# Kernel tuning notes

Measured on AMD Instinct MI355X. Metric: run time of the kernel, lower is better.

Reference implementation:

```python
import jax, jax.numpy as jnp
import numpy as np

B, E, W_WORDS, V = 512, 512, 64, 32000
H = 10 * E  # dense hidden = embedding_size * 10


def setup_inputs() -> dict:
    key = jax.random.key(0)
    ks = jax.random.split(key, 16)
    u = lambda k, shp: jax.random.uniform(ks[k], shp, jnp.float32, -0.05, 0.05)
    n = lambda k, shp: jax.random.normal(ks[k], shp, jnp.float32)
    return {
        "y": n(0, (B, E)),
        "state": n(1, (B, E)),
        "encode": n(2, (B, W_WORDS, E)),
        # Bahdanau attention weights (W4 unused in forward, omitted)
        "aW1": u(3, (1, E)),
        "aW2": u(4, (W_WORDS, E)),
        "aW3": u(5, (W_WORDS, E)),
        # Keras GRU (reset_after=True): kernel, recurrent_kernel, bias[2, 3E]
        "gk": u(6, (E, 3 * E)),
        "grk": u(7, (E, 3 * E)),
        "gb": u(8, (2, 3 * E)),
        # Dense stack
        "w1": u(9, (3 * E, H)), "b1": jnp.zeros((H,), jnp.float32),
        "w2": u(10, (H, H)), "b2": jnp.zeros((H,), jnp.float32),
        "w3": u(11, (H, V)), "b3": jnp.zeros((V,), jnp.float32),
    }


def _attention(query, value, aW1, aW2, aW3):
    # einsum('bi,ci->bi', query, W1) with c==1  ->  query * W1[0]
    rq = query * aW1[0]                       # [B, E]
    rv = value * aW2                          # [B, W, E] (broadcast over batch)
    s = jnp.tanh(rq[:, None, :] * rv)         # [B, W, E]
    scores = jnp.sum(s * aW3, axis=-1)        # [B, W]
    a = jax.nn.softmax(scores, axis=-1)       # [B, W]
    return jnp.einsum('bw,bwe->be', a, value)  # context [B, E]


def _gru(seq, gk, grk, gb):
    # seq: [T, B, E]; keras GRU defaults: tanh / sigmoid, reset_after=True, h0=0
    bi, br = gb[0], gb[1]

    def step(h, x):
        xz, xr, xh = jnp.split(x @ gk + bi, 3, axis=-1)
        rz, rr, rh = jnp.split(h @ grk + br, 3, axis=-1)
        z = jax.nn.sigmoid(xz + rz)
        r = jax.nn.sigmoid(xr + rr)
        hh = jnp.tanh(xh + r * rh)
        return z * h + (1.0 - z) * hh, None

    h0 = jnp.zeros(seq.shape[1:], seq.dtype)
    h, _ = jax.lax.scan(step, h0, seq)
    return h


def reference(y, state, encode, aW1, aW2, aW3, gk, grk, gb, w1, b1, w2, b2, w3, b3):
    context = _attention(state, encode, aW1, aW2, aW3)   # [B, E]
    seq = jnp.stack([state, context, y], axis=0)          # [3, B, E]
    new_state = _gru(seq, gk, grk, gb)                    # [B, E]
    g = jnp.concatenate([y, context, new_state], axis=-1)  # [B, 3E]
    h1 = jnp.tanh(g @ w1 + b1)
    h2 = jnp.tanh(h1 @ w2 + b2)
    g_output = jax.nn.softmax(h2 @ w3 + b3, axis=-1)      # [B, V]
    return (g_output, new_state)
```

## Files before the change

### kernel.cpp

```cpp
#include <hip/hip_runtime.h>
#include <hip/hip_bf16.h>
#include <math.h>

#define B_DIM 512
#define E_DIM 512
#define W_DIM 64
#define V_DIM 32000
#define H_DIM 5120

typedef short bf16x8 __attribute__((ext_vector_type(8)));
typedef float f32x4 __attribute__((ext_vector_type(4)));

static __device__ __forceinline__ unsigned pk2(float a, float b) {
  union { __hip_bfloat16 h; unsigned short u; } ca, cb;
  ca.h = __float2bfloat16(a);
  cb.h = __float2bfloat16(b);
  return (unsigned)ca.u | ((unsigned)cb.u << 16);
}
static __device__ __forceinline__ unsigned short f2b(float a) {
  union { __hip_bfloat16 h; unsigned short u; } c;
  c.h = __float2bfloat16(a);
  return c.u;
}

__global__ __launch_bounds__(256) void attn_kernel(
    const float* __restrict__ state, const float* __restrict__ encode,
    const float* __restrict__ aW1, const float* __restrict__ aW2,
    const float* __restrict__ aW3, float* __restrict__ ctx) {
  const int b = blockIdx.x;
  const int tid = threadIdx.x;
  __shared__ float rq[512];
  __shared__ float sc[64];
  rq[tid]       = state[(size_t)b * 512 + tid]       * aW1[tid];
  rq[tid + 256] = state[(size_t)b * 512 + tid + 256] * aW1[tid + 256];
  __syncthreads();
  const int lane = tid & 63, wv = tid >> 6;
  const float* enc = encode + (size_t)b * 64 * 512;
  for (int w = wv; w < 64; w += 4) {
    const float* er  = enc + w * 512;
    const float* w2r = aW2 + w * 512;
    const float* w3r = aW3 + w * 512;
    float s = 0.f;
#pragma unroll
    for (int k = 0; k < 8; ++k) {
      int e = lane + k * 64;
      s += tanhf(rq[e] * er[e] * w2r[e]) * w3r[e];
    }
#pragma unroll
    for (int o = 32; o; o >>= 1) s += __shfl_xor(s, o, 64);
    if (lane == 0) sc[w] = s;
  }
  __syncthreads();
  if (tid < 64) {
    float v = sc[tid];
    float mx = v;
#pragma unroll
    for (int o = 32; o; o >>= 1) mx = fmaxf(mx, __shfl_xor(mx, o, 64));
    float e = __expf(v - mx);
    float sm = e;
#pragma unroll
    for (int o = 32; o; o >>= 1) sm += __shfl_xor(sm, o, 64);
    sc[tid] = e / sm;
  }
  __syncthreads();
  for (int e = tid; e < 512; e += 256) {
    float acc = 0.f;
#pragma unroll 8
    for (int w = 0; w < 64; ++w) acc += sc[w] * enc[w * 512 + e];
    ctx[(size_t)b * 512 + e] = acc;
  }
}

__global__ __launch_bounds__(256) void pack3(
    const float* __restrict__ s0, const float* __restrict__ s1,
    const float* __restrict__ s2, float* __restrict__ dst) {
  const int s = blockIdx.y;
  const int i = blockIdx.x * 256 + threadIdx.x;
  const float* src = (s == 0) ? s0 : ((s == 1) ? s1 : s2);
  dst[(size_t)s * 262144 + i] = src[i];
}

__global__ __launch_bounds__(256) void pack3b(
    const float* __restrict__ s0, const float* __restrict__ s1,
    const float* __restrict__ s2, unsigned short* __restrict__ dst) {
  const int s = blockIdx.y;
  const int i = blockIdx.x * 256 + threadIdx.x;
  const float* src = (s == 0) ? s0 : ((s == 1) ? s1 : s2);
  const int b = i >> 9, e = i & 511;
  dst[(size_t)b * 1536 + s * 512 + e] = f2b(src[i]);
}

__global__ __launch_bounds__(256) void gru_gate(
    const float* __restrict__ X, const float* __restrict__ R, int rstride,
    const float* __restrict__ hprev, float* __restrict__ hout) {
  const int i = blockIdx.x * 256 + threadIdx.x;
  const int b = i >> 9, e = i & 511;
  const float* Xr = X + (size_t)b * 1536;
  const float* Rr = R + (size_t)b * rstride;
  const float xz = Xr[e], xr = Xr[512 + e], xh = Xr[1024 + e];
  const float rz = Rr[e], rr = Rr[512 + e], rh = Rr[1024 + e];
  const float h = hprev ? hprev[i] : 0.f;
  const float z = 1.f / (1.f + __expf(-(xz + rz)));
  const float r = 1.f / (1.f + __expf(-(xr + rr)));
  const float hh = tanhf(xh + r * rh);
  hout[i] = z * h + (1.f - z) * hh;
}

template <int ACT>
__global__ __launch_bounds__(256, 2) void gemm_k(
    const float* __restrict__ A, const float* __restrict__ B,
    const float* __restrict__ bias, float* __restrict__ C,
    int M, int N, int K) {
  __shared__ unsigned short As[128 * 72];
  __shared__ unsigned short Bs[128 * 72];
  const int tid = threadIdx.x;
  const int bid = blockIdx.x;
  const int tiles_m = M >> 7;
  const int mt = bid % tiles_m;
  const int nt = bid / tiles_m;
  const long m0 = (long)mt * 128, n0 = (long)nt * 128;

  const int a_m = tid & 127;
  const int a_h = tid >> 7;
  unsigned short* awp = As + a_m * 72 + a_h * 32;
  const int b_n = (tid & 31) << 2;
  const int b_q = (tid >> 5) & 3;
  const int b_h = tid >> 7;
  const int b_sw = ((b_q ^ (tid & 3)) << 3) + b_h * 32;

  const int lane = tid & 63;
  const int wid = tid >> 6;
  const int wm = (wid >> 1) << 6, wn = (wid & 1) << 6;
  const int lr = lane & 15, lg = lane >> 4;

  int aro[4], bro[4];
#pragma unroll
  for (int i = 0; i < 4; ++i)
    aro[i] = (wm + 16 * i + lr) * 72 + 8 * lg;
#pragma unroll
  for (int j = 0; j < 4; ++j) {
    const int n = wn + 16 * j + lr;
    bro[j] = n * 72 + 8 * (lg ^ ((n >> 2) & 3));
  }

  f32x4 acc[4][4];
#pragma unroll
  for (int i = 0; i < 4; ++i)
#pragma unroll
    for (int j = 0; j < 4; ++j) acc[i][j] = f32x4{0.f, 0.f, 0.f, 0.f};

  const float* ap = A + (m0 + a_m) * (long)K + a_h * 32;
  const float* bp = B + (size_t)(b_h * 32 + b_q * 8) * N + n0 + b_n;

  float4 pb[8];
#pragma unroll
  for (int j = 0; j < 8; ++j) pb[j] = *(const float4*)(bp + (size_t)j * N);
  bp += (size_t)64 * N;

  const int nsteps = K >> 6;
  for (int t = 0; t < nsteps; ++t) {
    float4 pa[8];
#pragma unroll
    for (int j = 0; j < 8; ++j) pa[j] = *(const float4*)(ap + 4 * j);
    ap += 64;
    {
      uint4 w;
      w.x = pk2(pb[0].x, pb[1].x); w.y = pk2(pb[2].x, pb[3].x);
      w.z = pk2(pb[4].x, pb[5].x); w.w = pk2(pb[6].x, pb[7].x);
      *(uint4*)(Bs + (b_n + 0) * 72 + b_sw) = w;
      w.x = pk2(pb[0].y, pb[1].y); w.y = pk2(pb[2].y, pb[3].y);
      w.z = pk2(pb[4].y, pb[5].y); w.w = pk2(pb[6].y, pb[7].y);
      *(uint4*)(Bs + (b_n + 1) * 72 + b_sw) = w;
      w.x = pk2(pb[0].z, pb[1].z); w.y = pk2(pb[2].z, pb[3].z);
      w.z = pk2(pb[4].z, pb[5].z); w.w = pk2(pb[6].z, pb[7].z);
      *(uint4*)(Bs + (b_n + 2) * 72 + b_sw) = w;
      w.x = pk2(pb[0].w, pb[1].w); w.y = pk2(pb[2].w, pb[3].w);
      w.z = pk2(pb[4].w, pb[5].w); w.w = pk2(pb[6].w, pb[7].w);
      *(uint4*)(Bs + (b_n + 3) * 72 + b_sw) = w;
    }
#pragma unroll
    for (int c = 0; c < 4; ++c) {
      uint4 w;
      w.x = pk2(pa[2 * c].x, pa[2 * c].y);
      w.y = pk2(pa[2 * c].z, pa[2 * c].w);
      w.z = pk2(pa[2 * c + 1].x, pa[2 * c + 1].y);
      w.w = pk2(pa[2 * c + 1].z, pa[2 * c + 1].w);
      *(uint4*)(awp + 8 * c) = w;
    }
    __syncthreads();
    if (t + 1 < nsteps) {
#pragma unroll
      for (int j = 0; j < 8; ++j) pb[j] = *(const float4*)(bp + (size_t)j * N);
      bp += (size_t)64 * N;
    }
#pragma unroll
    for (int s = 0; s < 2; ++s) {
      bf16x8 af[4], bfr[4];
#pragma unroll
      for (int i = 0; i < 4; ++i)
        af[i] = *(const bf16x8*)(As + aro[i] + 32 * s);
#pragma unroll
      for (int j = 0; j < 4; ++j)
        bfr[j] = *(const bf16x8*)(Bs + bro[j] + 32 * s);
#pragma unroll
      for (int i = 0; i < 4; ++i)
#pragma unroll
        for (int j = 0; j < 4; ++j)
          acc[i][j] = __builtin_amdgcn_mfma_f32_16x16x32_bf16(af[i], bfr[j], acc[i][j], 0, 0, 0);
    }
    __syncthreads();
  }
#pragma unroll
  for (int j = 0; j < 4; ++j) {
    const long col = n0 + wn + j * 16 + lr;
    const float bv = bias ? bias[col] : 0.f;
#pragma unroll
    for (int i = 0; i < 4; ++i) {
      const long row = m0 + wm + i * 16 + (lg << 2);
#pragma unroll
      for (int r = 0; r < 4; ++r) {
        float x = acc[i][j][r] + bv;
        if (ACT == 1) x = tanhf(x);
        C[(row + r) * N + col] = x;
      }
    }
  }
}

template <int ACT, int PARTS>
__global__ __launch_bounds__(512, 2) void gemm_pn(
    const unsigned short* __restrict__ A16, const float* __restrict__ B,
    const float* __restrict__ bias, float* __restrict__ C,
    int N, int K) {
  __shared__ unsigned short Bs[2][128 * 72];
  const int tid = threadIdx.x;
  const long n0 = (long)blockIdx.x * 128;
  const int Kp = K / PARTS;
  const int k0 = blockIdx.y * Kp;

  const int b_x = tid & 31;
  const int b_n = b_x << 2;
  const int b_g = tid >> 5;
  const int b_gs = (((b_g >> 1) ^ ((b_x >> 1) & 7)) << 1) | (b_g & 1);
  const int bw0 = (b_n + 0) * 72 + b_gs * 4;
  const int bw1 = (b_n + 1) * 72 + b_gs * 4;
  const int bw2 = (b_n + 2) * 72 + b_gs * 4;
  const int bw3 = (b_n + 3) * 72 + b_gs * 4;

  const int lane = tid & 63;
  const int wid = tid >> 6;
  const int wm = wid << 6;
  const int lr = lane & 15, lg = lane >> 4;

  int bbase[8], bslot[8];
#pragma unroll
  for (int j = 0; j < 8; ++j) {
    const int n = 16 * j + lr;
    bbase[j] = n * 72;
    bslot[j] = lg ^ ((n >> 3) & 7);
  }

  f32x4 acc[4][8];
#pragma unroll
  for (int i = 0; i < 4; ++i)
#pragma unroll
    for (int j = 0; j < 8; ++j) acc[i][j] = f32x4{0.f, 0.f, 0.f, 0.f};

  const unsigned short* ap0 = A16 + (size_t)(wm + lr) * K + k0 + 8 * lg;
  const unsigned short* ap1 = ap0 + (size_t)16 * K;
  const unsigned short* ap2 = ap0 + (size_t)32 * K;
  const unsigned short* ap3 = ap0 + (size_t)48 * K;
  const float* bp = B + (size_t)(k0 + b_g * 4) * N + n0 + b_n;

  float4 pb0, pb1, pb2, pb3;
  bf16x8 af[8];

#define LOAD_B()                                  \
  do {                                            \
    pb0 = *(const float4*)(bp);                   \
    pb1 = *(const float4*)(bp + N);               \
    pb2 = *(const float4*)(bp + 2 * (size_t)N);   \
    pb3 = *(const float4*)(bp + 3 * (size_t)N);   \
    bp += (size_t)64 * N;                         \
  } while (0)

#define LOAD_A()                                  \
  do {                                            \
    af[0] = *(const bf16x8*)(ap0);                \
    af[1] = *(const bf16x8*)(ap1);                \
    af[2] = *(const bf16x8*)(ap2);                \
    af[3] = *(const bf16x8*)(ap3);                \
    af[4] = *(const bf16x8*)(ap0 + 32);           \
    af[5] = *(const bf16x8*)(ap1 + 32);           \
    af[6] = *(const bf16x8*)(ap2 + 32);           \
    af[7] = *(const bf16x8*)(ap3 + 32);           \
    ap0 += 64; ap1 += 64; ap2 += 64; ap3 += 64;   \
  } while (0)

#define WRITE_B(buf)                                           \
  do {                                                         \
    uint2 qv;                                                  \
    qv.x = pk2(pb0.x, pb1.x); qv.y = pk2(pb2.x, pb3.x);        \
    *(uint2*)(Bs[buf] + bw0) = qv;                             \
    qv.x = pk2(pb0.y, pb1.y); qv.y = pk2(pb2.y, pb3.y);        \
    *(uint2*)(Bs[buf] + bw1) = qv;                             \
    qv.x = pk2(pb0.z, pb1.z); qv.y = pk2(pb2.z, pb3.z);        \
    *(uint2*)(Bs[buf] + bw2) = qv;                             \
    qv.x = pk2(pb0.w, pb1.w); qv.y = pk2(pb2.w, pb3.w);        \
    *(uint2*)(Bs[buf] + bw3) = qv;                             \
  } while (0)

  const int nsteps = Kp >> 6;
  LOAD_B();
  LOAD_A();
  WRITE_B(0);
  LOAD_B();
  asm volatile("s_waitcnt lgkmcnt(0)" ::: "memory");
  __builtin_amdgcn_s_barrier();

  for (int t = 0; t < nsteps; ++t) {
    const int buf = t & 1;
    if (t + 1 < nsteps) { WRITE_B(buf ^ 1); }
    if (t + 2 < nsteps) { LOAD_B(); }
#pragma unroll
    for (int s = 0; s < 2; ++s) {
      bf16x8 bfr[8];
#pragma unroll
      for (int j = 0; j < 8; ++j)
        bfr[j] = *(const bf16x8*)(Bs[buf] + bbase[j] + 8 * (bslot[j] ^ (s << 2)));
#pragma unroll
      for (int i = 0; i < 4; ++i)
#pragma unroll
        for (int j = 0; j < 8; ++j)
          acc[i][j] = __builtin_amdgcn_mfma_f32_16x16x32_bf16(
              af[s * 4 + i], bfr[j], acc[i][j], 0, 0, 0);
    }
    if (t + 1 < nsteps) { LOAD_A(); }
    asm volatile("s_waitcnt lgkmcnt(0)" ::: "memory");
    __builtin_amdgcn_s_barrier();
  }
#undef LOAD_B
#undef LOAD_A
#undef WRITE_B
  float* Cp = (PARTS > 1) ? (C + (size_t)blockIdx.y * 512 * (size_t)N) : C;
#pragma unroll
  for (int j = 0; j < 8; ++j) {
    const long col = n0 + 16 * j + lr;
    const float bv = (PARTS == 1 && bias) ? bias[col] : 0.f;
#pragma unroll
    for (int i = 0; i < 4; ++i) {
      const long row = wm + 16 * i + (lg << 2);
#pragma unroll
      for (int r = 0; r < 4; ++r) {
        float x = acc[i][j][r] + bv;
        if (PARTS == 1 && ACT == 1) x = tanhf(x);
        Cp[(row + r) * N + col] = x;
      }
    }
  }
}

template <int ACT, int PARTS>
__global__ __launch_bounds__(256) void reduce_parts_b(
    const float* __restrict__ P, const float* __restrict__ bias,
    unsigned short* __restrict__ dst, int N) {
  const int col = blockIdx.x * 256 + threadIdx.x;
  const int row = blockIdx.y;
  const size_t MN = (size_t)512 * N;
  const size_t idx = (size_t)row * N + col;
  float s = bias[col];
#pragma unroll
  for (int p = 0; p < PARTS; ++p) s += P[p * MN + idx];
  dst[idx] = f2b((ACT == 1) ? tanhf(s) : s);
}

__global__ __launch_bounds__(256) void softmax_rows(float* __restrict__ x) {
  const int b = blockIdx.x;
  float* row = x + (size_t)b * V_DIM;
  const int tid = threadIdx.x;
  __shared__ float red[4];
  const float4* r4 = (const float4*)row;
  float mx = -3.4e38f;
  for (int i = tid; i < V_DIM / 4; i += 256) {
    float4 v = r4[i];
    mx = fmaxf(mx, fmaxf(fmaxf(v.x, v.y), fmaxf(v.z, v.w)));
  }
#pragma unroll
  for (int o = 32; o; o >>= 1) mx = fmaxf(mx, __shfl_xor(mx, o, 64));
  if ((tid & 63) == 0) red[tid >> 6] = mx;
  __syncthreads();
  mx = fmaxf(fmaxf(red[0], red[1]), fmaxf(red[2], red[3]));
  __syncthreads();
  float s = 0.f;
  for (int i = tid; i < V_DIM / 4; i += 256) {
    float4 v = r4[i];
    s += __expf(v.x - mx) + __expf(v.y - mx) + __expf(v.z - mx) + __expf(v.w - mx);
  }
#pragma unroll
  for (int o = 32; o; o >>= 1) s += __shfl_xor(s, o, 64);
  if ((tid & 63) == 0) red[tid >> 6] = s;
  __syncthreads();
  s = red[0] + red[1] + red[2] + red[3];
  const float inv = 1.f / s;
  float4* w4p = (float4*)row;
  for (int i = tid; i < V_DIM / 4; i += 256) {
    float4 v = r4[i];
    float4 o4;
    o4.x = __expf(v.x - mx) * inv;
    o4.y = __expf(v.y - mx) * inv;
    o4.z = __expf(v.z - mx) * inv;
    o4.w = __expf(v.w - mx) * inv;
    w4p[i] = o4;
  }
}

extern "C" void kernel_launch(void* const* d_in, const int* in_sizes, int n_in,
                              void* d_out, int out_size, void* d_ws, size_t ws_size,
                              hipStream_t stream) {
  const float* y      = (const float*)d_in[0];
  const float* state  = (const float*)d_in[1];
  const float* encode = (const float*)d_in[2];
  const float* aW1    = (const float*)d_in[3];
  const float* aW2    = (const float*)d_in[4];
  const float* aW3    = (const float*)d_in[5];
  const float* gk     = (const float*)d_in[6];
  const float* grk    = (const float*)d_in[7];
  const float* gb     = (const float*)d_in[8];
  const float* w1     = (const float*)d_in[9];
  const float* b1     = (const float*)d_in[10];
  const float* w2     = (const float*)d_in[11];
  const float* b2     = (const float*)d_in[12];
  const float* w3     = (const float*)d_in[13];
  const float* b3     = (const float*)d_in[14];
  float* out = (float*)d_out;
  float* ws = (float*)d_ws;

  float* ctx = ws;
  float* seq = ws + 262144;
  float* X   = ws + 1048576;
  float* R   = ws + 3407872;
  float* hg1 = ws + 4194304;
  float* hg2 = ws + 4456448;
  unsigned short* gb16  = (unsigned short*)(ws + 4718592);
  unsigned short* dd1b  = (unsigned short*)(ws + 5111808);
  unsigned short* dd2b  = (unsigned short*)(ws + 6422528);

  float* g_out = out;
  float* h3 = out + (size_t)B_DIM * V_DIM;
  float* P = out;

  const float* bi = gb;
  const float* br = gb + 1536;

  attn_kernel<<<512, 256, 0, stream>>>(state, encode, aW1, aW2, aW3, ctx);
  pack3<<<dim3(1024, 3), 256, 0, stream>>>(state, ctx, y, seq);
  gemm_k<0><<<12 * 12, 256, 0, stream>>>(seq, gk, bi, X, 1536, 1536, 512);
  gru_gate<<<1024, 256, 0, stream>>>(X, br, 0, nullptr, hg1);
  gemm_k<0><<<4 * 12, 256, 0, stream>>>(hg1, grk, br, R, 512, 1536, 512);
  gru_gate<<<1024, 256, 0, stream>>>(X + 786432, R, 1536, hg1, hg2);
  gemm_k<0><<<4 * 12, 256, 0, stream>>>(hg2, grk, br, R, 512, 1536, 512);
  gru_gate<<<1024, 256, 0, stream>>>(X + 1572864, R, 1536, hg2, h3);
  pack3b<<<dim3(1024, 3), 256, 0, stream>>>(y, ctx, h3, gb16);
  gemm_pn<0, 6><<<dim3(40, 6), 512, 0, stream>>>(gb16, w1, nullptr, P, H_DIM, 1536);
  reduce_parts_b<1, 6><<<dim3(20, 512), 256, 0, stream>>>(P, b1, dd1b, H_DIM);
  gemm_pn<0, 5><<<dim3(40, 5), 512, 0, stream>>>(dd1b, w2, nullptr, P, H_DIM, H_DIM);
  reduce_parts_b<1, 5><<<dim3(20, 512), 256, 0, stream>>>(P, b2, dd2b, H_DIM);
  gemm_pn<0, 1><<<dim3(250, 1), 512, 0, stream>>>(dd2b, w3, b3, g_out, V_DIM, H_DIM);
  softmax_rows<<<512, 256, 0, stream>>>(g_out);
}
```

Measured before the change: 532.4 us.

## Split-K GRU GEMMs, drop seq pack, online softmax, split A loads

The GRU GEMMs now use a 2-way split-K grid that writes partial outputs, and the gate kernel sums them and adds the biases. This doubles the block count on the small 48-block recurrent GEMMs. The separate pack3 copy is removed: gemm_k picks its source rows directly from state/ctx/y. The output softmax merges the max and sum passes into one online pass, and gemm_pn splits its A-fragment reloads into two halves interleaved with the MFMA stages. In exchange, the partial buffers add extra memory traffic, and the online softmax computes more exponentials.

```diff
diff --git a/kernel.cpp b/kernel.cpp
--- a/kernel.cpp
+++ b/kernel.cpp
@@ -71,15 +71,6 @@
   }
 }
 
-__global__ __launch_bounds__(256) void pack3(
-    const float* __restrict__ s0, const float* __restrict__ s1,
-    const float* __restrict__ s2, float* __restrict__ dst) {
-  const int s = blockIdx.y;
-  const int i = blockIdx.x * 256 + threadIdx.x;
-  const float* src = (s == 0) ? s0 : ((s == 1) ? s1 : s2);
-  dst[(size_t)s * 262144 + i] = src[i];
-}
-
 __global__ __launch_bounds__(256) void pack3b(
     const float* __restrict__ s0, const float* __restrict__ s1,
     const float* __restrict__ s2, unsigned short* __restrict__ dst) {
@@ -91,14 +82,28 @@
 }
 
 __global__ __launch_bounds__(256) void gru_gate(
-    const float* __restrict__ X, const float* __restrict__ R, int rstride,
+    const float* __restrict__ X0, const float* __restrict__ X1,
+    const float* __restrict__ bi,
+    const float* __restrict__ R0, const float* __restrict__ R1,
+    const float* __restrict__ br,
     const float* __restrict__ hprev, float* __restrict__ hout) {
   const int i = blockIdx.x * 256 + threadIdx.x;
   const int b = i >> 9, e = i & 511;
-  const float* Xr = X + (size_t)b * 1536;
-  const float* Rr = R + (size_t)b * rstride;
-  const float xz = Xr[e], xr = Xr[512 + e], xh = Xr[1024 + e];
-  const float rz = Rr[e], rr = Rr[512 + e], rh = Rr[1024 + e];
+  const float* X0r = X0 + (size_t)b * 1536;
+  const float* X1r = X1 + (size_t)b * 1536;
+  const float xz = X0r[e]        + X1r[e]        + bi[e];
+  const float xr = X0r[512 + e]  + X1r[512 + e]  + bi[512 + e];
+  const float xh = X0r[1024 + e] + X1r[1024 + e] + bi[1024 + e];
+  float rz, rr, rh;
+  if (R0) {
+    const float* R0r = R0 + (size_t)b * 1536;
+    const float* R1r = R1 + (size_t)b * 1536;
+    rz = R0r[e]        + R1r[e]        + br[e];
+    rr = R0r[512 + e]  + R1r[512 + e]  + br[512 + e];
+    rh = R0r[1024 + e] + R1r[1024 + e] + br[1024 + e];
+  } else {
+    rz = br[e]; rr = br[512 + e]; rh = br[1024 + e];
+  }
   const float h = hprev ? hprev[i] : 0.f;
   const float z = 1.f / (1.f + __expf(-(xz + rz)));
   const float r = 1.f / (1.f + __expf(-(xr + rr)));
@@ -106,11 +111,11 @@
   hout[i] = z * h + (1.f - z) * hh;
 }
 
-template <int ACT>
+template <int PARTS>
 __global__ __launch_bounds__(256, 2) void gemm_k(
-    const float* __restrict__ A, const float* __restrict__ B,
-    const float* __restrict__ bias, float* __restrict__ C,
-    int M, int N, int K) {
+    const float* __restrict__ a0, const float* __restrict__ a1,
+    const float* __restrict__ a2, const float* __restrict__ B,
+    float* __restrict__ C, int M, int N, int K) {
   __shared__ unsigned short As[128 * 72];
   __shared__ unsigned short Bs[128 * 72];
   const int tid = threadIdx.x;
@@ -119,6 +124,8 @@
   const int mt = bid % tiles_m;
   const int nt = bid / tiles_m;
   const long m0 = (long)mt * 128, n0 = (long)nt * 128;
+  const int Kp = K / PARTS;
+  const int k0 = blockIdx.y * Kp;
 
   const int a_m = tid & 127;
   const int a_h = tid >> 7;
@@ -149,15 +156,17 @@
 #pragma unroll
     for (int j = 0; j < 4; ++j) acc[i][j] = f32x4{0.f, 0.f, 0.f, 0.f};
 
-  const float* ap = A + (m0 + a_m) * (long)K + a_h * 32;
-  const float* bp = B + (size_t)(b_h * 32 + b_q * 8) * N + n0 + b_n;
+  const int row = (int)m0 + a_m;
+  const float* asrc = (row < 512) ? a0 : ((row < 1024) ? a1 : a2);
+  const float* ap = asrc + (size_t)(row & 511) * 512 + k0 + a_h * 32;
+  const float* bp = B + (size_t)(k0 + b_h * 32 + b_q * 8) * N + n0 + b_n;
 
   float4 pb[8];
 #pragma unroll
   for (int j = 0; j < 8; ++j) pb[j] = *(const float4*)(bp + (size_t)j * N);
   bp += (size_t)64 * N;
 
-  const int nsteps = K >> 6;
+  const int nsteps = Kp >> 6;
   for (int t = 0; t < nsteps; ++t) {
     float4 pa[8];
 #pragma unroll
@@ -210,19 +219,16 @@
     }
     __syncthreads();
   }
+  float* Cp = (PARTS > 1) ? (C + (size_t)blockIdx.y * M * (size_t)N) : C;
 #pragma unroll
   for (int j = 0; j < 4; ++j) {
     const long col = n0 + wn + j * 16 + lr;
-    const float bv = bias ? bias[col] : 0.f;
 #pragma unroll
     for (int i = 0; i < 4; ++i) {
-      const long row = m0 + wm + i * 16 + (lg << 2);
-#pragma unroll
-      for (int r = 0; r < 4; ++r) {
-        float x = acc[i][j][r] + bv;
-        if (ACT == 1) x = tanhf(x);
-        C[(row + r) * N + col] = x;
-      }
+      const long row2 = m0 + wm + i * 16 + (lg << 2);
+#pragma unroll
+      for (int r = 0; r < 4; ++r)
+        Cp[(row2 + r) * N + col] = acc[i][j][r];
     }
   }
 }
@@ -284,12 +290,16 @@
     bp += (size_t)64 * N;                         \
   } while (0)
 
-#define LOAD_A()                                  \
+#define LOAD_A0()                                 \
   do {                                            \
     af[0] = *(const bf16x8*)(ap0);                \
     af[1] = *(const bf16x8*)(ap1);                \
     af[2] = *(const bf16x8*)(ap2);                \
     af[3] = *(const bf16x8*)(ap3);                \
+  } while (0)
+
+#define LOAD_A1()                                 \
+  do {                                            \
     af[4] = *(const bf16x8*)(ap0 + 32);           \
     af[5] = *(const bf16x8*)(ap1 + 32);           \
     af[6] = *(const bf16x8*)(ap2 + 32);           \
@@ -312,7 +322,8 @@
 
   const int nsteps = Kp >> 6;
   LOAD_B();
-  LOAD_A();
+  LOAD_A0();
+  LOAD_A1();
   WRITE_B(0);
   LOAD_B();
   asm volatile("s_waitcnt lgkmcnt(0)" ::: "memory");
@@ -322,25 +333,38 @@
     const int buf = t & 1;
     if (t + 1 < nsteps) { WRITE_B(buf ^ 1); }
     if (t + 2 < nsteps) { LOAD_B(); }
-#pragma unroll
-    for (int s = 0; s < 2; ++s) {
+    {
       bf16x8 bfr[8];
 #pragma unroll
       for (int j = 0; j < 8; ++j)
-        bfr[j] = *(const bf16x8*)(Bs[buf] + bbase[j] + 8 * (bslot[j] ^ (s << 2)));
+        bfr[j] = *(const bf16x8*)(Bs[buf] + bbase[j] + 8 * bslot[j]);
 #pragma unroll
       for (int i = 0; i < 4; ++i)
 #pragma unroll
         for (int j = 0; j < 8; ++j)
           acc[i][j] = __builtin_amdgcn_mfma_f32_16x16x32_bf16(
-              af[s * 4 + i], bfr[j], acc[i][j], 0, 0, 0);
-    }
-    if (t + 1 < nsteps) { LOAD_A(); }
+              af[i], bfr[j], acc[i][j], 0, 0, 0);
+    }
+    if (t + 1 < nsteps) { LOAD_A0(); }
+    {
+      bf16x8 bfr[8];
+#pragma unroll
+      for (int j = 0; j < 8; ++j)
+        bfr[j] = *(const bf16x8*)(Bs[buf] + bbase[j] + 8 * (bslot[j] ^ 4));
+#pragma unroll
+      for (int i = 0; i < 4; ++i)
+#pragma unroll
+        for (int j = 0; j < 8; ++j)
+          acc[i][j] = __builtin_amdgcn_mfma_f32_16x16x32_bf16(
+              af[4 + i], bfr[j], acc[i][j], 0, 0, 0);
+    }
+    if (t + 1 < nsteps) { LOAD_A1(); }
     asm volatile("s_waitcnt lgkmcnt(0)" ::: "memory");
     __builtin_amdgcn_s_barrier();
   }
 #undef LOAD_B
-#undef LOAD_A
+#undef LOAD_A0
+#undef LOAD_A1
 #undef WRITE_B
   float* Cp = (PARTS > 1) ? (C + (size_t)blockIdx.y * 512 * (size_t)N) : C;
 #pragma unroll
@@ -378,38 +402,38 @@
   const int b = blockIdx.x;
   float* row = x + (size_t)b * V_DIM;
   const int tid = threadIdx.x;
-  __shared__ float red[4];
+  const int lane = tid & 63, w = tid >> 6;
+  __shared__ float sm[4], sl[4];
   const float4* r4 = (const float4*)row;
-  float mx = -3.4e38f;
+  float m = -3.4e38f, l = 0.f;
   for (int i = tid; i < V_DIM / 4; i += 256) {
     float4 v = r4[i];
-    mx = fmaxf(mx, fmaxf(fmaxf(v.x, v.y), fmaxf(v.z, v.w)));
-  }
-#pragma unroll
-  for (int o = 32; o; o >>= 1) mx = fmaxf(mx, __shfl_xor(mx, o, 64));
-  if ((tid & 63) == 0) red[tid >> 6] = mx;
+    float cm = fmaxf(fmaxf(v.x, v.y), fmaxf(v.z, v.w));
+    if (cm > m) { l *= __expf(m - cm); m = cm; }
+    l += __expf(v.x - m) + __expf(v.y - m) + __expf(v.z - m) + __expf(v.w - m);
+  }
+#pragma unroll
+  for (int o = 32; o; o >>= 1) {
+    float om = __shfl_xor(m, o, 64);
+    float ol = __shfl_xor(l, o, 64);
+    float nm = fmaxf(m, om);
+    l = l * __expf(m - nm) + ol * __expf(om - nm);
+    m = nm;
+  }
+  if (lane == 0) { sm[w] = m; sl[w] = l; }
   __syncthreads();
-  mx = fmaxf(fmaxf(red[0], red[1]), fmaxf(red[2], red[3]));
-  __syncthreads();
-  float s = 0.f;
-  for (int i = tid; i < V_DIM / 4; i += 256) {
-    float4 v = r4[i];
-    s += __expf(v.x - mx) + __expf(v.y - mx) + __expf(v.z - mx) + __expf(v.w - mx);
-  }
-#pragma unroll
-  for (int o = 32; o; o >>= 1) s += __shfl_xor(s, o, 64);
-  if ((tid & 63) == 0) red[tid >> 6] = s;
-  __syncthreads();
-  s = red[0] + red[1] + red[2] + red[3];
-  const float inv = 1.f / s;
+  float M = fmaxf(fmaxf(sm[0], sm[1]), fmaxf(sm[2], sm[3]));
+  float L = sl[0] * __expf(sm[0] - M) + sl[1] * __expf(sm[1] - M) +
+            sl[2] * __expf(sm[2] - M) + sl[3] * __expf(sm[3] - M);
+  const float inv = 1.f / L;
   float4* w4p = (float4*)row;
   for (int i = tid; i < V_DIM / 4; i += 256) {
     float4 v = r4[i];
     float4 o4;
-    o4.x = __expf(v.x - mx) * inv;
-    o4.y = __expf(v.y - mx) * inv;
-    o4.z = __expf(v.z - mx) * inv;
-    o4.w = __expf(v.w - mx) * inv;
+    o4.x = __expf(v.x - M) * inv;
+    o4.y = __expf(v.y - M) * inv;
+    o4.z = __expf(v.z - M) * inv;
+    o4.w = __expf(v.w - M) * inv;
     w4p[i] = o4;
   }
 }
@@ -436,14 +460,15 @@
   float* ws = (float*)d_ws;
 
   float* ctx = ws;
-  float* seq = ws + 262144;
-  float* X   = ws + 1048576;
-  float* R   = ws + 3407872;
-  float* hg1 = ws + 4194304;
-  float* hg2 = ws + 4456448;
-  unsigned short* gb16  = (unsigned short*)(ws + 4718592);
-  unsigned short* dd1b  = (unsigned short*)(ws + 5111808);
-  unsigned short* dd2b  = (unsigned short*)(ws + 6422528);
+  float* X0  = ws + 262144;
+  float* X1  = ws + 2621440;
+  float* R0  = ws + 4980736;
+  float* R1  = ws + 5767168;
+  float* hg1 = ws + 6553600;
+  float* hg2 = ws + 6815744;
+  unsigned short* gb16 = (unsigned short*)(ws + 7077888);
+  unsigned short* dd1b = (unsigned short*)(ws + 7471104);
+  unsigned short* dd2b = (unsigned short*)(ws + 8781824);
 
   float* g_out = out;
   float* h3 = out + (size_t)B_DIM * V_DIM;
@@ -453,13 +478,12 @@
   const float* br = gb + 1536;
 
   attn_kernel<<<512, 256, 0, stream>>>(state, encode, aW1, aW2, aW3, ctx);
-  pack3<<<dim3(1024, 3), 256, 0, stream>>>(state, ctx, y, seq);
-  gemm_k<0><<<12 * 12, 256, 0, stream>>>(seq, gk, bi, X, 1536, 1536, 512);
-  gru_gate<<<1024, 256, 0, stream>>>(X, br, 0, nullptr, hg1);
-  gemm_k<0><<<4 * 12, 256, 0, stream>>>(hg1, grk, br, R, 512, 1536, 512);
-  gru_gate<<<1024, 256, 0, stream>>>(X + 786432, R, 1536, hg1, hg2);
-  gemm_k<0><<<4 * 12, 256, 0, stream>>>(hg2, grk, br, R, 512, 1536, 512);
-  gru_gate<<<1024, 256, 0, stream>>>(X + 1572864, R, 1536, hg2, h3);
+  gemm_k<2><<<dim3(12 * 12, 2), 256, 0, stream>>>(state, ctx, y, gk, X0, 1536, 1536, 512);
+  gru_gate<<<1024, 256, 0, stream>>>(X0, X1, bi, nullptr, nullptr, br, nullptr, hg1);
+  gemm_k<2><<<dim3(4 * 12, 2), 256, 0, stream>>>(hg1, hg1, hg1, grk, R0, 512, 1536, 512);
+  gru_gate<<<1024, 256, 0, stream>>>(X0 + 786432, X1 + 786432, bi, R0, R1, br, hg1, hg2);
+  gemm_k<2><<<dim3(4 * 12, 2), 256, 0, stream>>>(hg2, hg2, hg2, grk, R0, 512, 1536, 512);
+  gru_gate<<<1024, 256, 0, stream>>>(X0 + 1572864, X1 + 1572864, bi, R0, R1, br, hg2, h3);
   pack3b<<<dim3(1024, 3), 256, 0, stream>>>(y, ctx, h3, gb16);
   gemm_pn<0, 6><<<dim3(40, 6), 512, 0, stream>>>(gb16, w1, nullptr, P, H_DIM, 1536);
   reduce_parts_b<1, 6><<<dim3(20, 512), 256, 0, stream>>>(P, b1, dd1b, H_DIM);
```

Result: faster. 521.6 us (-2.0%).
